# Kernel tuning notes

Measured on AMD Instinct MI355X. Metric: run time of the kernel, lower is better.

The kernel has to match this reference:

```python
import jax, jax.numpy as jnp
import numpy as np

B, L, D = 8, 4096, 512
KS = (3, 5, 7)
EPS = 1e-5
W_SCALE = 0.02  # tame torch.randn-style init for numerical sanity


def layernorm(x, g, b):
    mu = jnp.mean(x, axis=-1, keepdims=True)
    var = jnp.var(x, axis=-1, keepdims=True)
    return (x - mu) * jax.lax.rsqrt(var + EPS) * g + b


def masked_conv(x1, chain, W, b):
    # x1: (B, C, L); W: (O, C, K); chain: (B, L) int32
    K = W.shape[2]
    pad_l = (K - 1) // 2
    pad_r = (K - 1) - pad_l
    xp = jnp.pad(x1, ((0, 0), (0, 0), (pad_l, pad_r)))
    ip = jnp.pad(chain, ((0, 0), (pad_l, pad_r)))  # pad id = 0
    Lx = x1.shape[2]
    # center tap of each window is the position's own chain id (odd K, center == pad_l)
    out = b[None, :, None]
    for k in range(K):  # small static loop over taps
        xs = xp[:, :, k:k + Lx]                      # (B, C, L)
        mk = (ip[:, k:k + Lx] == chain)              # (B, L) bool
        out = out + jnp.einsum('bcl,oc->bol', xs * mk[:, None, :], W[:, :, k])
    return out


def setup_inputs() -> dict:
    key = jax.random.key(0)
    ks = jax.random.split(key, 16)
    inp = {
        'x': jax.random.normal(ks[0], (B, L, D), dtype=jnp.float32),
        'chain': jnp.sort(jax.random.randint(ks[1], (B, L), 0, 8), axis=-1).astype(jnp.int32),
    }
    for i, (name, K) in enumerate(zip(('W3', 'W5', 'W7'), KS)):
        inp[name] = jax.random.normal(ks[2 + i], (D, D, K), dtype=jnp.float32) * W_SCALE
        inp['b' + name[1:]] = jax.random.normal(ks[5 + i], (D,), dtype=jnp.float32) * W_SCALE
    inp['mlp_w1'] = jax.random.normal(ks[8], (D, 4 * D), dtype=jnp.float32) * W_SCALE
    inp['mlp_b1'] = jnp.zeros((4 * D,), dtype=jnp.float32)
    inp['mlp_w2'] = jax.random.normal(ks[9], (4 * D, D), dtype=jnp.float32) * W_SCALE
    inp['mlp_b2'] = jnp.zeros((D,), dtype=jnp.float32)
    inp['ln1_g'] = jnp.ones((D,), dtype=jnp.float32)
    inp['ln1_b'] = jnp.zeros((D,), dtype=jnp.float32)
    inp['ln2_g'] = jnp.ones((D,), dtype=jnp.float32)
    inp['ln2_b'] = jnp.zeros((D,), dtype=jnp.float32)
    return inp


def reference(x, chain, W3, b3, W5, b5, W7, b7,
              mlp_w1, mlp_b1, mlp_w2, mlp_b2,
              ln1_g, ln1_b, ln2_g, ln2_b):
    x1 = jnp.transpose(x, (0, 2, 1))  # (B, C, L)
    for W, b in ((W3, b3), (W5, b5), (W7, b7)):
        x1 = masked_conv(x1, chain, W, b)
    h = layernorm(x + jnp.transpose(x1, (0, 2, 1)), ln1_g, ln1_b)
    mlp = jax.nn.gelu(h @ mlp_w1 + mlp_b1) @ mlp_w2 + mlp_b2
    return layernorm(h + mlp, ln2_g, ln2_b)
```

## Files before the change

kernel.cpp:

```cpp
#include <hip/hip_runtime.h>
#include <math.h>

#define BB 8
#define LL 4096
#define DD 512
#define PTOT (BB*LL)
#define HID  2048

typedef __attribute__((ext_vector_type(8))) short short8;
typedef __attribute__((ext_vector_type(4))) float f32x4;

typedef __attribute__((address_space(1))) const unsigned int gconst_u32;
typedef __attribute__((address_space(3))) unsigned int lds_u32;

__device__ __forceinline__ void gload16(const void* g, void* l) {
    __builtin_amdgcn_global_load_lds((gconst_u32*)g, (lds_u32*)l, 16, 0, 0);
}

__device__ __forceinline__ unsigned short f2bf(float f) {
    union { float f; unsigned int u; } v; v.f = f;
    unsigned int r = v.u + 0x7fffu + ((v.u >> 16) & 1u);
    return (unsigned short)(r >> 16);
}
__device__ __forceinline__ float bf2f(unsigned short h) {
    union { unsigned int u; float f; } v; v.u = ((unsigned int)h) << 16;
    return v.f;
}
__device__ __forceinline__ float gelu_fast(float x) {
    float x2 = x * x;
    float t  = x * fmaf(0.044715f, x2, 1.0f);
    float e  = __builtin_amdgcn_exp2f(-2.3021143f * t);
    return x * __builtin_amdgcn_rcpf(1.0f + e);
}

__global__ __launch_bounds__(256) void convert_x(const float* __restrict__ x,
                                                 unsigned short* __restrict__ xb) {
    int tid = blockIdx.x * 256 + threadIdx.x;
    float4 v = ((const float4*)x)[tid];
    uint2 o;
    o.x = (unsigned int)f2bf(v.x) | ((unsigned int)f2bf(v.y) << 16);
    o.y = (unsigned int)f2bf(v.z) | ((unsigned int)f2bf(v.w) << 16);
    ((uint2*)xb)[tid] = o;
}

__global__ __launch_bounds__(256) void trans_wconv(const float* __restrict__ W,
                                                   unsigned short* __restrict__ Wt, int K) {
    int tid = blockIdx.x * 256 + threadIdx.x;
    if (tid >= DD * DD * K) return;
    int o  = tid / (K * DD);
    int kc = tid - o * K * DD;
    int k  = kc >> 9;
    int c  = kc & (DD - 1);
    Wt[tid] = f2bf(W[(o * DD + c) * K + k]);
}

__global__ __launch_bounds__(256) void trans_w1(const float* __restrict__ W,
                                                unsigned short* __restrict__ Wt) {
    int tid = blockIdx.x * 256 + threadIdx.x;
    int n = tid >> 9;
    int c = tid & (DD - 1);
    Wt[tid] = f2bf(W[c * HID + n]);
}

__global__ __launch_bounds__(256) void trans_w2(const float* __restrict__ W,
                                                unsigned short* __restrict__ Wt) {
    int tid = blockIdx.x * 256 + threadIdx.x;
    int n = tid >> 11;
    int h = tid & (HID - 1);
    Wt[tid] = f2bf(W[h * DD + n]);
}

__global__ __launch_bounds__(256) void make_maskb(const int* __restrict__ chain,
                                                  unsigned char* __restrict__ mb,
                                                  unsigned short* __restrict__ zp) {
    int p = blockIdx.x * 256 + threadIdx.x;
    if (blockIdx.x == 0 && threadIdx.x < 128) zp[threadIdx.x] = 0;
    int b = p >> 12;
    int l = p & (LL - 1);
    int c0 = chain[p];
    unsigned m = 0;
#pragma unroll
    for (int d = -3; d <= 3; d++) {
        int l2 = l + d;
        bool ok = (l2 >= 0) && (l2 < LL) && (chain[b * LL + l2] == c0);
        m |= (ok ? 1u : 0u) << (d + 3);
    }
    mb[p] = (unsigned char)m;
}

template <int K>
__global__ __launch_bounds__(256, 3) void conv_mfma(
        const unsigned short* __restrict__ A,
        const unsigned char* __restrict__ maskb,
        const unsigned short* __restrict__ Bt,
        const float* __restrict__ bias,
        unsigned short* __restrict__ Y,
        const unsigned short* __restrict__ zp) {
    const int PAD = (K - 1) / 2;
    const int LDB = K * DD;
    __shared__ alignas(16) unsigned short As[144 * 64];
    __shared__ alignas(16) unsigned short Bs[2][128 * 64];

    int t = threadIdx.x;
    int p0 = blockIdx.x * 128;
    int o0 = blockIdx.y * 128;
    int w = t >> 6, lane = t & 63;
    int wr = w & 1, wc = w >> 1;
    int lm = lane & 15, q = lane >> 4;
    int lrow8 = lane >> 3;
    int qq = (lane & 7) ^ lrow8;

    unsigned int mbits[4];
#pragma unroll
    for (int mi = 0; mi < 4; mi++)
        mbits[mi] = maskb[p0 + wr * 64 + mi * 16 + lm];

    size_t brow[4];
#pragma unroll
    for (int j = 0; j < 4; j++)
        brow[j] = (size_t)(o0 + w * 32 + j * 8 + lrow8) * LDB + qq * 8;

    const unsigned short* agp[5];
    int nch = (w < 2) ? 5 : 4;
#pragma unroll
    for (int i = 0; i < 5; i++) {
        int c = (i < 4) ? (w + 4 * i) : (16 + w);
        int gr = p0 - 8 + c * 8 + lrow8;
        agp[i] = (gr >= 0 && gr < PTOT) ? (A + (size_t)gr * DD + qq * 8) : zp;
    }

    f32x4 acc[4][4];
#pragma unroll
    for (int mi = 0; mi < 4; mi++)
#pragma unroll
        for (int nj = 0; nj < 4; nj++) acc[mi][nj] = (f32x4){0.f, 0.f, 0.f, 0.f};

    for (int kc = 0; kc < DD; kc += 64) {
        for (int i = 0; i < nch; i++) {
            int c = (i < 4) ? (w + 4 * i) : (16 + w);
            const unsigned short* g = agp[i];
            gload16((g == zp) ? g : (g + kc), As + c * 512);
        }
#pragma unroll
        for (int j = 0; j < 4; j++)
            gload16(Bt + brow[j] + kc, Bs[0] + w * 2048 + j * 512);
        __syncthreads();

        for (int tap = 0; tap < K; tap++) {
            int cur = tap & 1;
            if (tap + 1 < K) {
#pragma unroll
                for (int j = 0; j < 4; j++)
                    gload16(Bt + brow[j] + (size_t)(tap + 1) * DD + kc,
                            Bs[cur ^ 1] + w * 2048 + j * 512);
            }
            int d  = tap - PAD;
            int mb = tap - PAD + 3;
            bool keep[4];
#pragma unroll
            for (int mi = 0; mi < 4; mi++) keep[mi] = (mbits[mi] >> mb) & 1;
            int rm = (lm + d) & 7;

#pragma unroll
            for (int kk = 0; kk < 2; kk++) {
                int slot = kk * 4 + q;
                int sab = (slot ^ (lm & 7)) * 8;
                int saa = (slot ^ rm) * 8;
                short8 b[4];
#pragma unroll
                for (int nj = 0; nj < 4; nj++)
                    b[nj] = *(const short8*)&Bs[cur][(wc * 64 + nj * 16 + lm) * 64 + sab];
#pragma unroll
                for (int mi = 0; mi < 4; mi++) {
                    int hr = 8 + wr * 64 + mi * 16 + lm + d;
                    short8 a = *(const short8*)&As[hr * 64 + saa];
                    short8 zero = {};
                    a = keep[mi] ? a : zero;
#pragma unroll
                    for (int nj = 0; nj < 4; nj++)
                        acc[mi][nj] = __builtin_amdgcn_mfma_f32_16x16x32_bf16(
                            a, b[nj], acc[mi][nj], 0, 0, 0);
                }
            }
            __syncthreads();
        }
    }

#pragma unroll
    for (int mi = 0; mi < 4; mi++) {
#pragma unroll
        for (int nj = 0; nj < 4; nj++) {
            int col = o0 + wc * 64 + nj * 16 + lm;
#pragma unroll
            for (int r = 0; r < 4; r++) {
                int row = p0 + wr * 64 + mi * 16 + q * 4 + r;
                Y[(size_t)row * DD + col] = f2bf(acc[mi][nj][r] + bias[col]);
            }
        }
    }
}

template <int EPI>
__global__ __launch_bounds__(256, 3) void mfma_gemm(
        const unsigned short* __restrict__ A, int lda,
        const unsigned short* __restrict__ Bt, int ldb,
        const float* __restrict__ bias,
        void* __restrict__ Yv, int ldc, int Kspan) {
    __shared__ alignas(16) unsigned short As[128 * 64];
    __shared__ alignas(16) unsigned short Bs[128 * 64];

    int t = threadIdx.x;
    int p0 = blockIdx.x * 128;
    int o0 = blockIdx.y * 128;
    int w = t >> 6, lane = t & 63;
    int wr = w & 1, wc = w >> 1;
    int lm = lane & 15, q = lane >> 4;
    int lrow8 = lane >> 3;
    int qq = (lane & 7) ^ lrow8;

    unsigned short* a_dst = As + w * 2048;
    unsigned short* b_dst = Bs + w * 2048;

    int aoff[4], boff[4];
#pragma unroll
    for (int i = 0; i < 4; i++) {
        aoff[i] = (p0 + w * 32 + i * 8 + lrow8) * lda + qq * 8;
        boff[i] = (o0 + w * 32 + i * 8 + lrow8) * ldb + qq * 8;
    }

    f32x4 acc[4][4];
#pragma unroll
    for (int mi = 0; mi < 4; mi++)
#pragma unroll
        for (int nj = 0; nj < 4; nj++) acc[mi][nj] = (f32x4){0.f, 0.f, 0.f, 0.f};

    for (int kc = 0; kc < Kspan; kc += 64) {
#pragma unroll
        for (int i = 0; i < 4; i++) {
            gload16(A + aoff[i] + kc, a_dst + i * 512);
            gload16(Bt + boff[i] + kc, b_dst + i * 512);
        }
        __syncthreads();
#pragma unroll
        for (int kk = 0; kk < 2; kk++) {
            int sa = ((kk * 4 + q) ^ (lm & 7)) * 8;
            short8 b[4];
#pragma unroll
            for (int nj = 0; nj < 4; nj++)
                b[nj] = *(const short8*)&Bs[(wc * 64 + nj * 16 + lm) * 64 + sa];
#pragma unroll
            for (int mi = 0; mi < 4; mi++) {
                short8 a = *(const short8*)&As[(wr * 64 + mi * 16 + lm) * 64 + sa];
#pragma unroll
                for (int nj = 0; nj < 4; nj++)
                    acc[mi][nj] = __builtin_amdgcn_mfma_f32_16x16x32_bf16(
                        a, b[nj], acc[mi][nj], 0, 0, 0);
            }
        }
        __syncthreads();
    }

#pragma unroll
    for (int mi = 0; mi < 4; mi++) {
#pragma unroll
        for (int nj = 0; nj < 4; nj++) {
            int col = o0 + wc * 64 + nj * 16 + lm;
#pragma unroll
            for (int r = 0; r < 4; r++) {
                int row = p0 + wr * 64 + mi * 16 + q * 4 + r;
                float v = acc[mi][nj][r];
                size_t idx = (size_t)row * ldc + col;
                if (EPI == 1) {
                    ((unsigned short*)Yv)[idx] = f2bf(gelu_fast(v + bias[col]));
                } else if (EPI == 2) {
                    ((float*)Yv)[idx] = v + bias[col];
                } else {
                    ((float*)Yv)[idx] += v;
                }
            }
        }
    }
}

__global__ __launch_bounds__(256) void ln1_kernel(const float* __restrict__ x,
                                                  const unsigned short* __restrict__ conv,
                                                  const float* __restrict__ g,
                                                  const float* __restrict__ beta,
                                                  unsigned short* __restrict__ h) {
    int p = blockIdx.x, t = threadIdx.x;
    size_t base = (size_t)p * DD;
    float v0 = x[base + t] + bf2f(conv[base + t]);
    float v1 = x[base + 256 + t] + bf2f(conv[base + 256 + t]);
    float s = v0 + v1, sq = v0 * v0 + v1 * v1;
#pragma unroll
    for (int off = 32; off > 0; off >>= 1) { s += __shfl_xor(s, off); sq += __shfl_xor(sq, off); }
    __shared__ float red[2][4];
    int wid = t >> 6, lane = t & 63;
    if (lane == 0) { red[0][wid] = s; red[1][wid] = sq; }
    __syncthreads();
    float S = red[0][0] + red[0][1] + red[0][2] + red[0][3];
    float SQ = red[1][0] + red[1][1] + red[1][2] + red[1][3];
    float mu = S * (1.f / DD);
    float var = SQ * (1.f / DD) - mu * mu;
    float rs = rsqrtf(var + 1e-5f);
    h[base + t]       = f2bf((v0 - mu) * rs * g[t] + beta[t]);
    h[base + 256 + t] = f2bf((v1 - mu) * rs * g[256 + t] + beta[256 + t]);
}

__global__ __launch_bounds__(256) void ln2_kernel(const unsigned short* __restrict__ h,
                                                  float* __restrict__ out,
                                                  const float* __restrict__ g,
                                                  const float* __restrict__ beta) {
    int p = blockIdx.x, t = threadIdx.x;
    size_t base = (size_t)p * DD;
    float v0 = bf2f(h[base + t]) + out[base + t];
    float v1 = bf2f(h[base + 256 + t]) + out[base + 256 + t];
    float s = v0 + v1, sq = v0 * v0 + v1 * v1;
#pragma unroll
    for (int off = 32; off > 0; off >>= 1) { s += __shfl_xor(s, off); sq += __shfl_xor(sq, off); }
    __shared__ float red[2][4];
    int wid = t >> 6, lane = t & 63;
    if (lane == 0) { red[0][wid] = s; red[1][wid] = sq; }
    __syncthreads();
    float S = red[0][0] + red[0][1] + red[0][2] + red[0][3];
    float SQ = red[1][0] + red[1][1] + red[1][2] + red[1][3];
    float mu = S * (1.f / DD);
    float var = SQ * (1.f / DD) - mu * mu;
    float rs = rsqrtf(var + 1e-5f);
    out[base + t]       = (v0 - mu) * rs * g[t] + beta[t];
    out[base + 256 + t] = (v1 - mu) * rs * g[256 + t] + beta[256 + t];
}

extern "C" void kernel_launch(void* const* d_in, const int* in_sizes, int n_in,
                              void* d_out, int out_size, void* d_ws, size_t ws_size,
                              hipStream_t stream) {
    const float* x     = (const float*)d_in[0];
    const int*   chain = (const int*)d_in[1];
    const float* W3    = (const float*)d_in[2];
    const float* b3    = (const float*)d_in[3];
    const float* W5    = (const float*)d_in[4];
    const float* b5    = (const float*)d_in[5];
    const float* W7    = (const float*)d_in[6];
    const float* b7    = (const float*)d_in[7];
    const float* w1    = (const float*)d_in[8];
    const float* bm1   = (const float*)d_in[9];
    const float* w2    = (const float*)d_in[10];
    const float* bm2   = (const float*)d_in[11];
    const float* g1    = (const float*)d_in[12];
    const float* be1   = (const float*)d_in[13];
    const float* g2    = (const float*)d_in[14];
    const float* be2   = (const float*)d_in[15];
    float* out = (float*)d_out;

    const size_t ACT = (size_t)PTOT * DD * 2;
    char* ws = (char*)d_ws;
    size_t off = 0;
    unsigned short* Xb   = (unsigned short*)(ws + off); off += ACT;
    unsigned short* buf1 = (unsigned short*)(ws + off); off += ACT;
    unsigned short* buf2 = (unsigned short*)(ws + off); off += ACT;
    unsigned short* w3t  = (unsigned short*)(ws + off); off += (size_t)3 * DD * DD * 2;
    unsigned short* w5t  = (unsigned short*)(ws + off); off += (size_t)5 * DD * DD * 2;
    unsigned short* w7t  = (unsigned short*)(ws + off); off += (size_t)7 * DD * DD * 2;
    unsigned short* w1t  = (unsigned short*)(ws + off); off += (size_t)DD * HID * 2;
    unsigned short* w2t  = (unsigned short*)(ws + off); off += (size_t)DD * HID * 2;
    unsigned char* maskb = (unsigned char*)(ws + off); off += PTOT;
    unsigned short* zp   = (unsigned short*)(ws + off); off += 256;
    size_t base_off = off;
    bool full = (ws_size >= base_off + (size_t)PTOT * HID * 2);
    unsigned short* Hb = (unsigned short*)(ws + base_off);

    convert_x<<<PTOT * DD / (256 * 4), 256, 0, stream>>>(x, Xb);
    trans_wconv<<<(DD * DD * 3 + 255) / 256, 256, 0, stream>>>(W3, w3t, 3);
    trans_wconv<<<(DD * DD * 5 + 255) / 256, 256, 0, stream>>>(W5, w5t, 5);
    trans_wconv<<<(DD * DD * 7 + 255) / 256, 256, 0, stream>>>(W7, w7t, 7);
    trans_w1<<<DD * HID / 256, 256, 0, stream>>>(w1, w1t);
    trans_w2<<<DD * HID / 256, 256, 0, stream>>>(w2, w2t);
    make_maskb<<<PTOT / 256, 256, 0, stream>>>(chain, maskb, zp);

    dim3 gconv(PTOT / 128, DD / 128);

    conv_mfma<3><<<gconv, 256, 0, stream>>>(Xb, maskb, w3t, b3, buf1, zp);
    conv_mfma<5><<<gconv, 256, 0, stream>>>(buf1, maskb, w5t, b5, buf2, zp);
    conv_mfma<7><<<gconv, 256, 0, stream>>>(buf2, maskb, w7t, b7, buf1, zp);

    ln1_kernel<<<PTOT, 256, 0, stream>>>(x, buf1, g1, be1, buf2);

    if (full) {
        dim3 g1d(PTOT / 128, HID / 128);
        mfma_gemm<1><<<g1d, 256, 0, stream>>>(buf2, DD, w1t, DD, bm1, Hb, HID, DD);
        mfma_gemm<2><<<gconv, 256, 0, stream>>>(Hb, HID, w2t, HID, bm2, out, DD, HID);
    } else {
        for (int jc = 0; jc < 4; jc++) {
            mfma_gemm<1><<<gconv, 256, 0, stream>>>(buf2, DD, w1t + (size_t)jc * DD * DD,
                                                    DD, bm1 + jc * DD, Hb, DD, DD);
            if (jc == 0)
                mfma_gemm<2><<<gconv, 256, 0, stream>>>(Hb, DD, w2t + jc * DD, HID, bm2,
                                                        out, DD, DD);
            else
                mfma_gemm<3><<<gconv, 256, 0, stream>>>(Hb, DD, w2t + jc * DD, HID, bm2,
                                                        out, DD, DD);
        }
    }

    ln2_kernel<<<PTOT, 256, 0, stream>>>(buf2, out, g2, be2);
}
```

Before: 708.7 us.

## Load weight fragments directly from global, double-buffer activation tiles, swap grid order

```diff
diff --git a/kernel.cpp b/kernel.cpp
--- a/kernel.cpp
+++ b/kernel.cpp
@@ -98,12 +98,11 @@
         const unsigned short* __restrict__ zp) {
     const int PAD = (K - 1) / 2;
     const int LDB = K * DD;
-    __shared__ alignas(16) unsigned short As[144 * 64];
-    __shared__ alignas(16) unsigned short Bs[2][128 * 64];
+    __shared__ alignas(16) unsigned short As[2][144 * 64];
 
     int t = threadIdx.x;
-    int p0 = blockIdx.x * 128;
-    int o0 = blockIdx.y * 128;
+    int o0 = blockIdx.x * 128;
+    int p0 = blockIdx.y * 128;
     int w = t >> 6, lane = t & 63;
     int wr = w & 1, wc = w >> 1;
     int lm = lane & 15, q = lane >> 4;
@@ -115,10 +114,10 @@
     for (int mi = 0; mi < 4; mi++)
         mbits[mi] = maskb[p0 + wr * 64 + mi * 16 + lm];
 
-    size_t brow[4];
-#pragma unroll
-    for (int j = 0; j < 4; j++)
-        brow[j] = (size_t)(o0 + w * 32 + j * 8 + lrow8) * LDB + qq * 8;
+    size_t bbase[4];
+#pragma unroll
+    for (int nj = 0; nj < 4; nj++)
+        bbase[nj] = (size_t)(o0 + wc * 64 + nj * 16 + lm) * LDB + q * 8;
 
     const unsigned short* agp[5];
     int nch = (w < 2) ? 5 : 4;
@@ -135,55 +134,57 @@
 #pragma unroll
         for (int nj = 0; nj < 4; nj++) acc[mi][nj] = (f32x4){0.f, 0.f, 0.f, 0.f};
 
+    for (int i = 0; i < nch; i++) {
+        int c = (i < 4) ? (w + 4 * i) : (16 + w);
+        const unsigned short* g = agp[i];
+        gload16(g, As[0] + c * 512);
+    }
+
+    int cur = 0;
     for (int kc = 0; kc < DD; kc += 64) {
-        for (int i = 0; i < nch; i++) {
-            int c = (i < 4) ? (w + 4 * i) : (16 + w);
-            const unsigned short* g = agp[i];
-            gload16((g == zp) ? g : (g + kc), As + c * 512);
-        }
-#pragma unroll
-        for (int j = 0; j < 4; j++)
-            gload16(Bt + brow[j] + kc, Bs[0] + w * 2048 + j * 512);
         __syncthreads();
-
+        if (kc + 64 < DD) {
+            for (int i = 0; i < nch; i++) {
+                int c = (i < 4) ? (w + 4 * i) : (16 + w);
+                const unsigned short* g = agp[i];
+                gload16((g == zp) ? g : (g + kc + 64), As[cur ^ 1] + c * 512);
+            }
+        }
+        const unsigned short* asrc = As[cur];
+
+#pragma unroll
         for (int tap = 0; tap < K; tap++) {
-            int cur = tap & 1;
-            if (tap + 1 < K) {
-#pragma unroll
-                for (int j = 0; j < 4; j++)
-                    gload16(Bt + brow[j] + (size_t)(tap + 1) * DD + kc,
-                            Bs[cur ^ 1] + w * 2048 + j * 512);
-            }
             int d  = tap - PAD;
-            int mb = tap - PAD + 3;
             bool keep[4];
 #pragma unroll
-            for (int mi = 0; mi < 4; mi++) keep[mi] = (mbits[mi] >> mb) & 1;
+            for (int mi = 0; mi < 4; mi++) keep[mi] = (mbits[mi] >> (d + 3)) & 1;
             int rm = (lm + d) & 7;
 
+            short8 bf[2][4];
+#pragma unroll
+            for (int kk = 0; kk < 2; kk++)
+#pragma unroll
+                for (int nj = 0; nj < 4; nj++)
+                    bf[kk][nj] = *(const short8*)(Bt + bbase[nj]
+                                   + (size_t)tap * DD + kc + kk * 32);
+
 #pragma unroll
             for (int kk = 0; kk < 2; kk++) {
-                int slot = kk * 4 + q;
-                int sab = (slot ^ (lm & 7)) * 8;
-                int saa = (slot ^ rm) * 8;
-                short8 b[4];
-#pragma unroll
-                for (int nj = 0; nj < 4; nj++)
-                    b[nj] = *(const short8*)&Bs[cur][(wc * 64 + nj * 16 + lm) * 64 + sab];
+                int saa = ((kk * 4 + q) ^ rm) * 8;
 #pragma unroll
                 for (int mi = 0; mi < 4; mi++) {
                     int hr = 8 + wr * 64 + mi * 16 + lm + d;
-                    short8 a = *(const short8*)&As[hr * 64 + saa];
+                    short8 a = *(const short8*)&asrc[hr * 64 + saa];
                     short8 zero = {};
                     a = keep[mi] ? a : zero;
 #pragma unroll
                     for (int nj = 0; nj < 4; nj++)
                         acc[mi][nj] = __builtin_amdgcn_mfma_f32_16x16x32_bf16(
-                            a, b[nj], acc[mi][nj], 0, 0, 0);
+                            a, bf[kk][nj], acc[mi][nj], 0, 0, 0);
                 }
             }
-            __syncthreads();
-        }
+        }
+        cur ^= 1;
     }
 
 #pragma unroll
@@ -206,27 +207,26 @@
         const unsigned short* __restrict__ Bt, int ldb,
         const float* __restrict__ bias,
         void* __restrict__ Yv, int ldc, int Kspan) {
-    __shared__ alignas(16) unsigned short As[128 * 64];
-    __shared__ alignas(16) unsigned short Bs[128 * 64];
+    __shared__ alignas(16) unsigned short As[2][128 * 64];
 
     int t = threadIdx.x;
-    int p0 = blockIdx.x * 128;
-    int o0 = blockIdx.y * 128;
+    int o0 = blockIdx.x * 128;
+    int p0 = blockIdx.y * 128;
     int w = t >> 6, lane = t & 63;
     int wr = w & 1, wc = w >> 1;
     int lm = lane & 15, q = lane >> 4;
     int lrow8 = lane >> 3;
     int qq = (lane & 7) ^ lrow8;
 
-    unsigned short* a_dst = As + w * 2048;
-    unsigned short* b_dst = Bs + w * 2048;
-
-    int aoff[4], boff[4];
-#pragma unroll
-    for (int i = 0; i < 4; i++) {
+    int aoff[4];
+#pragma unroll
+    for (int i = 0; i < 4; i++)
         aoff[i] = (p0 + w * 32 + i * 8 + lrow8) * lda + qq * 8;
-        boff[i] = (o0 + w * 32 + i * 8 + lrow8) * ldb + qq * 8;
-    }
+
+    size_t bbase[4];
+#pragma unroll
+    for (int nj = 0; nj < 4; nj++)
+        bbase[nj] = (size_t)(o0 + wc * 64 + nj * 16 + lm) * ldb + q * 8;
 
     f32x4 acc[4][4];
 #pragma unroll
@@ -234,30 +234,40 @@
 #pragma unroll
         for (int nj = 0; nj < 4; nj++) acc[mi][nj] = (f32x4){0.f, 0.f, 0.f, 0.f};
 
+#pragma unroll
+    for (int i = 0; i < 4; i++)
+        gload16(A + aoff[i], As[0] + w * 2048 + i * 512);
+
+    int cur = 0;
     for (int kc = 0; kc < Kspan; kc += 64) {
-#pragma unroll
-        for (int i = 0; i < 4; i++) {
-            gload16(A + aoff[i] + kc, a_dst + i * 512);
-            gload16(Bt + boff[i] + kc, b_dst + i * 512);
-        }
         __syncthreads();
+        if (kc + 64 < Kspan) {
+#pragma unroll
+            for (int i = 0; i < 4; i++)
+                gload16(A + aoff[i] + kc + 64, As[cur ^ 1] + w * 2048 + i * 512);
+        }
+        const unsigned short* asrc = As[cur];
+
+        short8 bf[2][4];
+#pragma unroll
+        for (int kk = 0; kk < 2; kk++)
+#pragma unroll
+            for (int nj = 0; nj < 4; nj++)
+                bf[kk][nj] = *(const short8*)(Bt + bbase[nj] + kc + kk * 32);
+
 #pragma unroll
         for (int kk = 0; kk < 2; kk++) {
             int sa = ((kk * 4 + q) ^ (lm & 7)) * 8;
-            short8 b[4];
-#pragma unroll
-            for (int nj = 0; nj < 4; nj++)
-                b[nj] = *(const short8*)&Bs[(wc * 64 + nj * 16 + lm) * 64 + sa];
 #pragma unroll
             for (int mi = 0; mi < 4; mi++) {
-                short8 a = *(const short8*)&As[(wr * 64 + mi * 16 + lm) * 64 + sa];
+                short8 a = *(const short8*)&asrc[(wr * 64 + mi * 16 + lm) * 64 + sa];
 #pragma unroll
                 for (int nj = 0; nj < 4; nj++)
                     acc[mi][nj] = __builtin_amdgcn_mfma_f32_16x16x32_bf16(
-                        a, b[nj], acc[mi][nj], 0, 0, 0);
+                        a, bf[kk][nj], acc[mi][nj], 0, 0, 0);
             }
         }
-        __syncthreads();
+        cur ^= 1;
     }
 
 #pragma unroll
@@ -377,7 +387,7 @@
     trans_w2<<<DD * HID / 256, 256, 0, stream>>>(w2, w2t);
     make_maskb<<<PTOT / 256, 256, 0, stream>>>(chain, maskb, zp);
 
-    dim3 gconv(PTOT / 128, DD / 128);
+    dim3 gconv(DD / 128, PTOT / 128);
 
     conv_mfma<3><<<gconv, 256, 0, stream>>>(Xb, maskb, w3t, b3, buf1, zp);
     conv_mfma<5><<<gconv, 256, 0, stream>>>(buf1, maskb, w5t, b5, buf2, zp);
@@ -386,7 +396,7 @@
     ln1_kernel<<<PTOT, 256, 0, stream>>>(x, buf1, g1, be1, buf2);
 
     if (full) {
-        dim3 g1d(PTOT / 128, HID / 128);
+        dim3 g1d(HID / 128, PTOT / 128);
         mfma_gemm<1><<<g1d, 256, 0, stream>>>(buf2, DD, w1t, DD, bm1, Hb, HID, DD);
         mfma_gemm<2><<<gconv, 256, 0, stream>>>(Hb, HID, w2t, HID, bm2, out, DD, HID);
     } else {
```

Result: slower. 1.017 ms (+43.5%).
